# Performance work log

Measured on AMD Instinct MI355X. Metric: run time of the kernel, lower is better.

The kernel has to match this reference:

```python
import jax, jax.numpy as jnp
import numpy as np

IMG_SIZE = 416.0
CLASS_NUM = 80
NUM_ANCH = 3
MAX_GT = 64  # fixed padding for per-image valid GT boxes (original uses a variable-size python loop)


def _bce_logits(x, t):
    # BCEWithLogits, elementwise: softplus(x) - x*t  (numerically stable)
    return jax.nn.softplus(x) - x * t


def _make_noobj_mask(pred_boxes, targets):
    # pred_boxes: [B,G,G,3,4] in pixel units; targets: [B,G,G,3,85]
    B, G = pred_boxes.shape[0], pred_boxes.shape[1]
    N = G * G * NUM_ANCH
    conf = targets[..., 4].reshape(B, N)
    boxes = targets[..., 0:4].reshape(B, N, 4)
    # gather up to MAX_GT ground-truth boxes per image (conf>0 are the valid ones)
    top_conf, idx = jax.lax.top_k(conf, MAX_GT)            # [B,M]
    gt = jnp.take_along_axis(boxes, idx[..., None], axis=1)  # [B,M,4]
    valid = top_conf > 0.0                                   # [B,M]

    p = pred_boxes.reshape(B, N, 4)
    pxy = p[:, :, None, 0:2]   # [B,N,1,2]
    pwh = p[:, :, None, 2:4]
    gxy = gt[:, None, :, 0:2]  # [B,1,M,2]
    gwh = gt[:, None, :, 2:4]

    imin = jnp.maximum(pxy - pwh / 2, gxy - gwh / 2)
    imax = jnp.minimum(pxy + pwh / 2, gxy + gwh / 2)
    iwh = jnp.maximum(imax - imin, 0.0)
    inter = iwh[..., 0] * iwh[..., 1]                        # [B,N,M]
    area_p = pwh[..., 0] * pwh[..., 1]
    area_g = gwh[..., 0] * gwh[..., 1]
    iou = inter / (area_p + area_g - inter + 1e-9)
    iou = jnp.where(valid[:, None, :], iou, 0.0)
    best_iou = jnp.max(iou, axis=-1)                         # [B,N]
    noobj = (best_iou < 0.6).astype(pred_boxes.dtype)
    return noobj.reshape(B, G, G, NUM_ANCH)


def reference(preds, targets, anchors):
    B, G = preds.shape[0], preds.shape[1]
    ratio = IMG_SIZE / G
    p = preds.reshape(B, G, G, NUM_ANCH, 5 + CLASS_NUM)
    box_xy_raw, box_wh_raw, conf_logit, cls_logit = jnp.split(p, [2, 4, 5], axis=-1)

    # grid offsets: offset[i,j] = (j, i)
    gx, gy = jnp.meshgrid(jnp.arange(G, dtype=preds.dtype), jnp.arange(G, dtype=preds.dtype))
    offset = jnp.stack([gx, gy], axis=-1).reshape(G, G, 1, 2)

    sig_xy = jax.nn.sigmoid(box_xy_raw)
    box_xy = (sig_xy + offset) * ratio                 # pixel units
    box_wh = jnp.exp(box_wh_raw) * anchors             # (anchors/ratio)*ratio = anchors
    pred_boxes = jnp.concatenate([box_xy, box_wh], axis=-1)

    preds_xy = box_xy / ratio - offset                 # == sig_xy
    true_xy = targets[..., 0:2] / ratio - offset
    true_wh = targets[..., 2:4] / anchors
    preds_wh = box_wh / anchors
    true_wh = jnp.where(true_wh == 0.0, 1.0, true_wh)
    preds_wh = jnp.where(preds_wh == 0.0, 1.0, preds_wh)
    true_wh = jnp.log(jnp.clip(true_wh, 1e-9, 1e9))
    preds_wh = jnp.log(jnp.clip(preds_wh, 1e-9, 1e9))

    obj = (targets[..., 4] > 0.0).astype(preds.dtype)  # [B,G,G,3]
    obj_e = obj[..., None]
    scale = 2.0 - targets[..., 2:3] / IMG_SIZE * targets[..., 3:4] / IMG_SIZE  # [B,G,G,3,1]

    txty_loss = jnp.sum(obj_e * (preds_xy - true_xy) ** 2 * scale) / B
    twth_loss = jnp.sum(obj_e * (preds_wh - true_wh) ** 2 * scale) / B

    noobj = _make_noobj_mask(pred_boxes, targets)      # [B,G,G,3]
    noobj_conf_mask = (1.0 - obj) * noobj
    conf_t = targets[..., 4:5]
    noobj_conf_loss = jnp.sum(noobj_conf_mask[..., None] * _bce_logits(conf_logit, conf_t)) / B
    obj_conf_loss = jnp.sum(obj_e * _bce_logits(conf_logit, conf_t)) / B
    class_loss = jnp.sum(obj_e * _bce_logits(cls_logit, targets[..., 5:])) / B

    total_loss = txty_loss + twth_loss + noobj_conf_loss + obj_conf_loss + class_loss
    return (txty_loss, twth_loss, noobj_conf_loss, obj_conf_loss, class_loss, total_loss)


def setup_inputs() -> dict:
    key = jax.random.key(0)
    ks = jax.random.split(key, 5)
    B, G, A, C = 32, 52, NUM_ANCH, CLASS_NUM
    N = G * G * A
    M_OBJ = 40  # GT boxes per image (< MAX_GT)
    preds = jax.random.normal(ks[0], (B, G, G, A * (5 + C)), jnp.float32) * 0.5
    idx = jax.random.randint(ks[1], (B, M_OBJ), 0, N)
    xy = jax.random.uniform(ks[2], (B, M_OBJ, 2), jnp.float32, 0.0, IMG_SIZE)
    wh = jax.random.uniform(ks[3], (B, M_OBJ, 2), jnp.float32, 16.0, 128.0)
    cid = jax.random.randint(ks[4], (B, M_OBJ), 0, C)
    onehot = jax.nn.one_hot(cid, C, dtype=jnp.float32)
    vals = jnp.concatenate([xy, wh, jnp.ones((B, M_OBJ, 1), jnp.float32), onehot], axis=-1)
    t = jnp.zeros((B, N, 5 + C), jnp.float32)
    t = t.at[jnp.arange(B)[:, None], idx].set(vals)
    targets = t.reshape(B, G, G, A, 5 + C)
    anchors = jnp.array([[10.0, 13.0], [16.0, 30.0], [33.0, 23.0]], jnp.float32)
    return {"preds": preds, "targets": targets, "anchors": anchors}
```

## Files before the change

### kernel.cpp

```cpp
#include <hip/hip_runtime.h>
#include <math.h>

#define GSZ 52
#define NA 3
#define NCLS 80
#define CH 85
#define NCA (GSZ*GSZ*NA)
#define MAXGT 64
#define RPB 32
#define FPT (RPB*CH)
#define F4PT (FPT/4)
#define MCHUNK 32

__device__ __forceinline__ float softplus_fast(float x) {
    return fmaxf(x, 0.0f) + __logf(1.0f + __expf(-fabsf(x)));
}

__global__ void k_init(int* cnt, int B) {
    if (threadIdx.x < B) cnt[threadIdx.x] = 0;
}

__global__ void k_tp(const float* __restrict__ tg, const float* __restrict__ pr,
                     const float* __restrict__ anchors, int* cnt,
                     float4* __restrict__ gtbox, int2* __restrict__ gtinfo,
                     float4* __restrict__ boxout, float* __restrict__ confout) {
    __shared__ float sT[FPT];
    __shared__ float sP[FPT];
    int tid = threadIdx.x;
    size_t rec0 = (size_t)blockIdx.x * RPB;

    {
        const float4* srcT = (const float4*)(tg + rec0 * CH);
        const float4* srcP = (const float4*)(pr + rec0 * CH);
        float4* dT = (float4*)sT;
        float4* dP = (float4*)sP;
        for (int i = tid; i < F4PT; i += 256) {
            dT[i] = srcT[i];
            dP[i] = srcP[i];
        }
    }
    __syncthreads();

    if (tid < RPB) {
        const float* r = sT + tid * CH;
        float conf = r[4];
        if (conf > 0.0f) {
            size_t glob = rec0 + tid;
            int b    = (int)(glob / NCA);
            int nloc = (int)(glob - (size_t)b * NCA);
            int cid = 0;
            for (int c = 0; c < NCLS; c++) if (r[5 + c] > 0.5f) cid = c;
            int pos = atomicAdd(cnt + b, 1);
            if (pos < MAXGT) {
                gtbox[b * MAXGT + pos]  = make_float4(r[0], r[1], r[2], r[3]);
                gtinfo[b * MAXGT + pos] = make_int2(nloc, cid);
            }
        }
    } else if (tid >= 64 && tid < 64 + RPB) {
        int t = tid - 64;
        const float* r = sP + t * CH;
        size_t glob = rec0 + t;
        int b    = (int)(glob / NCA);
        int nloc = (int)(glob - (size_t)b * NCA);
        int a    = nloc % NA;
        int cell = nloc / NA;
        int gi = cell / GSZ, gj = cell % GSZ;
        float sx = __builtin_amdgcn_rcpf(1.0f + __expf(-r[0]));
        float sy = __builtin_amdgcn_rcpf(1.0f + __expf(-r[1]));
        float ew = __expf(r[2]), eh = __expf(r[3]);
        float aw = anchors[2 * a], ah = anchors[2 * a + 1];
        boxout[glob] = make_float4((sx + (float)gj) * 8.0f,
                                   (sy + (float)gi) * 8.0f,
                                   ew * aw, eh * ah);
        confout[glob] = r[4];
    }
}

__global__ void k_main(const int* __restrict__ cnt,
                       const float4* __restrict__ gtbox,
                       const int2* __restrict__ gtinfo,
                       const float4* __restrict__ boxin,
                       const float* __restrict__ confin,
                       float* __restrict__ partial) {
    __shared__ float4 sbox[MAXGT];
    __shared__ int    sidx[MAXGT];
    __shared__ float  swsum[4];

    int b   = blockIdx.y;
    int tid = threadIdx.x;
    int n   = blockIdx.x * 256 + tid;

    int m = min(cnt[b], MAXGT);
    if (tid < m) {
        sbox[tid] = gtbox[b * MAXGT + tid];
        sidx[tid] = gtinfo[b * MAXGT + tid].x;
    }
    __syncthreads();

    float v = 0.0f;
    if (n < NCA) {
        size_t rec = (size_t)b * NCA + n;
        float4 pb = boxin[rec];
        float  pc = confin[rec];
        float px0 = pb.x - pb.z * 0.5f, px1 = pb.x + pb.z * 0.5f;
        float py0 = pb.y - pb.w * 0.5f, py1 = pb.y + pb.w * 0.5f;
        float areap = pb.z * pb.w;

        float best = 0.0f;
        bool isobj = false;
        for (int k = 0; k < m; k++) {
            float4 g = sbox[k];
            isobj |= (sidx[k] == n);
            float ix = fminf(px1, g.x + g.z * 0.5f) - fmaxf(px0, g.x - g.z * 0.5f);
            float iy = fminf(py1, g.y + g.w * 0.5f) - fmaxf(py0, g.y - g.w * 0.5f);
            float inter = fmaxf(ix, 0.0f) * fmaxf(iy, 0.0f);
            float u = areap + g.z * g.w - inter + 1e-9f;
            best = fmaxf(best, inter * __builtin_amdgcn_rcpf(u));
        }
        if (!isobj && best < 0.6f) v = softplus_fast(pc);
    }

    int lane = tid & 63;
    int wv   = tid >> 6;
    for (int off = 32; off > 0; off >>= 1) v += __shfl_down(v, off);
    if (lane == 0) swsum[wv] = v;
    __syncthreads();
    if (tid == 0) {
        int bid = blockIdx.y * gridDim.x + blockIdx.x;
        partial[bid] = swsum[0] + swsum[1] + swsum[2] + swsum[3];
    }
}

__global__ void k_cls(const float* __restrict__ pr,
                      const float* __restrict__ anchors,
                      const int* __restrict__ cnt,
                      const float4* __restrict__ gtbox,
                      const int2* __restrict__ gtinfo,
                      const float4* __restrict__ boxin,
                      const float* __restrict__ confin,
                      float4* __restrict__ cls4) {
    int tid  = threadIdx.x;
    int wv   = tid >> 6;
    int lane = tid & 63;
    int slot = blockIdx.x * 4 + wv;
    int b = slot >> 6;
    int k = slot & (MAXGT - 1);

    float4 resv = make_float4(0.f, 0.f, 0.f, 0.f);
    int m = min(cnt[b], MAXGT);
    if (k < m) {
        float4 g  = gtbox[slot];
        int2 info = gtinfo[slot];
        int n = info.x, cid = info.y;
        size_t rec = (size_t)b * NCA + n;
        const float* cl = pr + rec * CH + 5;

        float x0 = cl[lane];
        float cls = softplus_fast(x0) - (lane == cid ? x0 : 0.0f);
        if (lane < NCLS - 64) {
            float x1 = cl[64 + lane];
            cls += softplus_fast(x1) - ((64 + lane) == cid ? x1 : 0.0f);
        }
        for (int off = 32; off > 0; off >>= 1) cls += __shfl_down(cls, off);

        if (lane == 0) {
            float4 pb = boxin[rec];
            float  pc = confin[rec];
            int a    = n % NA;
            int cell = n / NA;
            int gi = cell / GSZ, gj = cell % GSZ;
            float aw = anchors[2 * a], ah = anchors[2 * a + 1];

            float scale = 2.0f - (g.z * (1.0f / 416.0f)) * (g.w * (1.0f / 416.0f));
            float dx = (pb.x * 0.125f - (float)gj) - (g.x * 0.125f - (float)gj);
            float dy = (pb.y * 0.125f - (float)gi) - (g.y * 0.125f - (float)gi);
            float txty = (dx * dx + dy * dy) * scale;

            float rw = __builtin_amdgcn_rcpf(aw), rh = __builtin_amdgcn_rcpf(ah);
            float pwr = fminf(fmaxf(pb.z * rw, 1e-9f), 1e9f);
            float phr = fminf(fmaxf(pb.w * rh, 1e-9f), 1e9f);
            float twr = fminf(fmaxf(g.z  * rw, 1e-9f), 1e9f);
            float thr = fminf(fmaxf(g.w  * rh, 1e-9f), 1e9f);
            float dw = __logf(pwr) - __logf(twr);
            float dh = __logf(phr) - __logf(thr);
            float twth = (dw * dw + dh * dh) * scale;

            float obj = softplus_fast(pc) - pc;
            resv = make_float4(txty, twth, obj, cls);
        }
    }
    if (lane == 0) cls4[slot] = resv;
}

__global__ void k_final(const float* __restrict__ partial, int np,
                        const float4* __restrict__ cls4, int ns,
                        int B, float* __restrict__ out) {
    __shared__ double sred[4 * 5];
    int tid = threadIdx.x;
    double acc[5] = {0, 0, 0, 0, 0};
    for (int i = tid; i < np; i += 256) acc[2] += (double)partial[i];
    for (int i = tid; i < ns; i += 256) {
        float4 v = cls4[i];
        acc[0] += (double)v.x; acc[1] += (double)v.y;
        acc[3] += (double)v.z; acc[4] += (double)v.w;
    }
    int lane = tid & 63;
    int wv   = tid >> 6;
#pragma unroll
    for (int i = 0; i < 5; i++) {
        double v = acc[i];
        for (int off = 32; off > 0; off >>= 1) v += __shfl_down(v, off);
        if (lane == 0) sred[wv * 5 + i] = v;
    }
    __syncthreads();
    if (tid == 0) {
        double tot = 0.0;
#pragma unroll
        for (int i = 0; i < 5; i++) {
            double r = (sred[i] + sred[5 + i] + sred[10 + i] + sred[15 + i]) / (double)B;
            out[i] = (float)r;
            tot += r;
        }
        out[5] = (float)tot;
    }
}

extern "C" void kernel_launch(void* const* d_in, const int* in_sizes, int n_in,
                              void* d_out, int out_size, void* d_ws, size_t ws_size,
                              hipStream_t stream) {
    const float* preds   = (const float*)d_in[0];
    const float* targets = (const float*)d_in[1];
    const float* anchors = (const float*)d_in[2];
    float* out = (float*)d_out;

    int B = in_sizes[0] / (NCA * CH);
    size_t total_rec = (size_t)B * NCA;
    int tp_blocks = (int)(total_rec / RPB);
    int np = MCHUNK * B;
    int ns = B * MAXGT;

    char* ws = (char*)d_ws;
    size_t off = 0;
    int*    cnt     = (int*)(ws + off);      off += 128;
    float4* gtbox   = (float4*)(ws + off);   off += (size_t)ns * sizeof(float4);
    int2*   gtinfo  = (int2*)(ws + off);     off += (size_t)ns * sizeof(int2);
    float*  partial = (float*)(ws + off);    off += (size_t)np * sizeof(float);
    off = (off + 15) & ~(size_t)15;
    float4* cls4    = (float4*)(ws + off);   off += (size_t)ns * sizeof(float4);
    float4* boxout  = (float4*)(ws + off);   off += total_rec * sizeof(float4);
    float*  confout = (float*)(ws + off);    off += total_rec * sizeof(float);

    k_init<<<1, 64, 0, stream>>>(cnt, B);
    k_tp<<<tp_blocks, 256, 0, stream>>>(targets, preds, anchors, cnt,
                                        gtbox, gtinfo, boxout, confout);
    dim3 grid(MCHUNK, B);
    k_main<<<grid, 256, 0, stream>>>(cnt, gtbox, gtinfo, boxout, confout, partial);
    k_cls<<<ns / 4, 256, 0, stream>>>(preds, anchors, cnt, gtbox, gtinfo,
                                      boxout, confout, cls4);
    k_final<<<1, 256, 0, stream>>>(partial, np, cls4, ns, B, out);
}
```

Measured before the change: 215.9 us.

## Drop full-tensor staging; read only conf channel and recompute boxes in consumers

The combined transform kernel, which staged every targets and preds record through shared memory, is split up. A new GT-scan kernel reads only the conf channel of targets and touches the full record only for positives. The noobj and class kernels now decode boxes from preds directly, so the intermediate box and conf buffers go away. The aim is to stop streaming both 85-channel tensors in full. The cost is strided 4-byte reads (one per 340-byte record), which use far fewer bytes but make poorly coalesced accesses, plus some duplicated sigmoid and exp work.

```diff
diff --git a/kernel.cpp b/kernel.cpp
--- a/kernel.cpp
+++ b/kernel.cpp
@@ -7,9 +7,6 @@
 #define CH 85
 #define NCA (GSZ*GSZ*NA)
 #define MAXGT 64
-#define RPB 32
-#define FPT (RPB*CH)
-#define F4PT (FPT/4)
 #define MCHUNK 32
 
 __device__ __forceinline__ float softplus_fast(float x) {
@@ -20,68 +17,39 @@
     if (threadIdx.x < B) cnt[threadIdx.x] = 0;
 }
 
-__global__ void k_tp(const float* __restrict__ tg, const float* __restrict__ pr,
-                     const float* __restrict__ anchors, int* cnt,
-                     float4* __restrict__ gtbox, int2* __restrict__ gtinfo,
-                     float4* __restrict__ boxout, float* __restrict__ confout) {
-    __shared__ float sT[FPT];
-    __shared__ float sP[FPT];
+__device__ __forceinline__ void emit_gt(const float* __restrict__ tg, size_t glob,
+                                        int* cnt, float4* __restrict__ gtbox,
+                                        int2* __restrict__ gtinfo) {
+    const float* r = tg + glob * CH;
+    int b    = (int)(glob / NCA);
+    int nloc = (int)(glob - (size_t)b * NCA);
+    int cid = 0;
+#pragma unroll 16
+    for (int c = 0; c < NCLS; c++) if (r[5 + c] > 0.5f) cid = c;
+    int pos = atomicAdd(cnt + b, 1);
+    if (pos < MAXGT) {
+        gtbox[b * MAXGT + pos]  = make_float4(r[0], r[1], r[2], r[3]);
+        gtinfo[b * MAXGT + pos] = make_int2(nloc, cid);
+    }
+}
+
+__global__ void k_gt(const float* __restrict__ tg, int nrec, int* cnt,
+                     float4* __restrict__ gtbox, int2* __restrict__ gtinfo) {
     int tid = threadIdx.x;
-    size_t rec0 = (size_t)blockIdx.x * RPB;
-
-    {
-        const float4* srcT = (const float4*)(tg + rec0 * CH);
-        const float4* srcP = (const float4*)(pr + rec0 * CH);
-        float4* dT = (float4*)sT;
-        float4* dP = (float4*)sP;
-        for (int i = tid; i < F4PT; i += 256) {
-            dT[i] = srcT[i];
-            dP[i] = srcP[i];
-        }
-    }
-    __syncthreads();
-
-    if (tid < RPB) {
-        const float* r = sT + tid * CH;
-        float conf = r[4];
-        if (conf > 0.0f) {
-            size_t glob = rec0 + tid;
-            int b    = (int)(glob / NCA);
-            int nloc = (int)(glob - (size_t)b * NCA);
-            int cid = 0;
-            for (int c = 0; c < NCLS; c++) if (r[5 + c] > 0.5f) cid = c;
-            int pos = atomicAdd(cnt + b, 1);
-            if (pos < MAXGT) {
-                gtbox[b * MAXGT + pos]  = make_float4(r[0], r[1], r[2], r[3]);
-                gtinfo[b * MAXGT + pos] = make_int2(nloc, cid);
-            }
-        }
-    } else if (tid >= 64 && tid < 64 + RPB) {
-        int t = tid - 64;
-        const float* r = sP + t * CH;
-        size_t glob = rec0 + t;
-        int b    = (int)(glob / NCA);
-        int nloc = (int)(glob - (size_t)b * NCA);
-        int a    = nloc % NA;
-        int cell = nloc / NA;
-        int gi = cell / GSZ, gj = cell % GSZ;
-        float sx = __builtin_amdgcn_rcpf(1.0f + __expf(-r[0]));
-        float sy = __builtin_amdgcn_rcpf(1.0f + __expf(-r[1]));
-        float ew = __expf(r[2]), eh = __expf(r[3]);
-        float aw = anchors[2 * a], ah = anchors[2 * a + 1];
-        boxout[glob] = make_float4((sx + (float)gj) * 8.0f,
-                                   (sy + (float)gi) * 8.0f,
-                                   ew * aw, eh * ah);
-        confout[glob] = r[4];
-    }
-}
-
-__global__ void k_main(const int* __restrict__ cnt,
-                       const float4* __restrict__ gtbox,
-                       const int2* __restrict__ gtinfo,
-                       const float4* __restrict__ boxin,
-                       const float* __restrict__ confin,
-                       float* __restrict__ partial) {
+    size_t g0 = (size_t)blockIdx.x * 512 + tid;
+    size_t g1 = g0 + 256;
+    float c0 = (g0 < (size_t)nrec) ? tg[g0 * CH + 4] : 0.0f;
+    float c1 = (g1 < (size_t)nrec) ? tg[g1 * CH + 4] : 0.0f;
+    if (c0 > 0.0f) emit_gt(tg, g0, cnt, gtbox, gtinfo);
+    if (c1 > 0.0f) emit_gt(tg, g1, cnt, gtbox, gtinfo);
+}
+
+__global__ void k_noobj(const float* __restrict__ pr,
+                        const float* __restrict__ anchors,
+                        const int* __restrict__ cnt,
+                        const float4* __restrict__ gtbox,
+                        const int2* __restrict__ gtinfo,
+                        float* __restrict__ partial) {
     __shared__ float4 sbox[MAXGT];
     __shared__ int    sidx[MAXGT];
     __shared__ float  swsum[4];
@@ -99,12 +67,23 @@
 
     float v = 0.0f;
     if (n < NCA) {
-        size_t rec = (size_t)b * NCA + n;
-        float4 pb = boxin[rec];
-        float  pc = confin[rec];
-        float px0 = pb.x - pb.z * 0.5f, px1 = pb.x + pb.z * 0.5f;
-        float py0 = pb.y - pb.w * 0.5f, py1 = pb.y + pb.w * 0.5f;
-        float areap = pb.z * pb.w;
+        const float* r = pr + ((size_t)b * NCA + n) * CH;
+        float r0 = r[0], r1 = r[1], r2 = r[2], r3 = r[3], pc = r[4];
+
+        int a    = n % NA;
+        int cell = n / NA;
+        int gi = cell / GSZ, gj = cell % GSZ;
+        float aw = anchors[2 * a], ah = anchors[2 * a + 1];
+        float sx = __builtin_amdgcn_rcpf(1.0f + __expf(-r0));
+        float sy = __builtin_amdgcn_rcpf(1.0f + __expf(-r1));
+        float bx = (sx + (float)gj) * 8.0f;
+        float by = (sy + (float)gi) * 8.0f;
+        float bw = __expf(r2) * aw;
+        float bh = __expf(r3) * ah;
+
+        float px0 = bx - bw * 0.5f, px1 = bx + bw * 0.5f;
+        float py0 = by - bh * 0.5f, py1 = by + bh * 0.5f;
+        float areap = bw * bh;
 
         float best = 0.0f;
         bool isobj = false;
@@ -136,8 +115,6 @@
                       const int* __restrict__ cnt,
                       const float4* __restrict__ gtbox,
                       const int2* __restrict__ gtinfo,
-                      const float4* __restrict__ boxin,
-                      const float* __restrict__ confin,
                       float4* __restrict__ cls4) {
     int tid  = threadIdx.x;
     int wv   = tid >> 6;
@@ -153,7 +130,8 @@
         int2 info = gtinfo[slot];
         int n = info.x, cid = info.y;
         size_t rec = (size_t)b * NCA + n;
-        const float* cl = pr + rec * CH + 5;
+        const float* rp = pr + rec * CH;
+        const float* cl = rp + 5;
 
         float x0 = cl[lane];
         float cls = softplus_fast(x0) - (lane == cid ? x0 : 0.0f);
@@ -164,21 +142,27 @@
         for (int off = 32; off > 0; off >>= 1) cls += __shfl_down(cls, off);
 
         if (lane == 0) {
-            float4 pb = boxin[rec];
-            float  pc = confin[rec];
+            float r0 = rp[0], r1 = rp[1], r2 = rp[2], r3 = rp[3], pc = rp[4];
             int a    = n % NA;
             int cell = n / NA;
             int gi = cell / GSZ, gj = cell % GSZ;
             float aw = anchors[2 * a], ah = anchors[2 * a + 1];
 
+            float sx = __builtin_amdgcn_rcpf(1.0f + __expf(-r0));
+            float sy = __builtin_amdgcn_rcpf(1.0f + __expf(-r1));
+            float pbx = (sx + (float)gj) * 8.0f;
+            float pby = (sy + (float)gi) * 8.0f;
+            float pbz = __expf(r2) * aw;
+            float pbw = __expf(r3) * ah;
+
             float scale = 2.0f - (g.z * (1.0f / 416.0f)) * (g.w * (1.0f / 416.0f));
-            float dx = (pb.x * 0.125f - (float)gj) - (g.x * 0.125f - (float)gj);
-            float dy = (pb.y * 0.125f - (float)gi) - (g.y * 0.125f - (float)gi);
+            float dx = (pbx * 0.125f - (float)gj) - (g.x * 0.125f - (float)gj);
+            float dy = (pby * 0.125f - (float)gi) - (g.y * 0.125f - (float)gi);
             float txty = (dx * dx + dy * dy) * scale;
 
             float rw = __builtin_amdgcn_rcpf(aw), rh = __builtin_amdgcn_rcpf(ah);
-            float pwr = fminf(fmaxf(pb.z * rw, 1e-9f), 1e9f);
-            float phr = fminf(fmaxf(pb.w * rh, 1e-9f), 1e9f);
+            float pwr = fminf(fmaxf(pbz * rw, 1e-9f), 1e9f);
+            float phr = fminf(fmaxf(pbw * rh, 1e-9f), 1e9f);
             float twr = fminf(fmaxf(g.z  * rw, 1e-9f), 1e9f);
             float thr = fminf(fmaxf(g.w  * rh, 1e-9f), 1e9f);
             float dw = __logf(pwr) - __logf(twr);
@@ -234,8 +218,8 @@
     float* out = (float*)d_out;
 
     int B = in_sizes[0] / (NCA * CH);
-    size_t total_rec = (size_t)B * NCA;
-    int tp_blocks = (int)(total_rec / RPB);
+    int nrec = B * NCA;
+    int gt_blocks = (nrec + 511) / 512;
     int np = MCHUNK * B;
     int ns = B * MAXGT;
 
@@ -247,15 +231,11 @@
     float*  partial = (float*)(ws + off);    off += (size_t)np * sizeof(float);
     off = (off + 15) & ~(size_t)15;
     float4* cls4    = (float4*)(ws + off);   off += (size_t)ns * sizeof(float4);
-    float4* boxout  = (float4*)(ws + off);   off += total_rec * sizeof(float4);
-    float*  confout = (float*)(ws + off);    off += total_rec * sizeof(float);
 
     k_init<<<1, 64, 0, stream>>>(cnt, B);
-    k_tp<<<tp_blocks, 256, 0, stream>>>(targets, preds, anchors, cnt,
-                                        gtbox, gtinfo, boxout, confout);
+    k_gt<<<gt_blocks, 256, 0, stream>>>(targets, nrec, cnt, gtbox, gtinfo);
     dim3 grid(MCHUNK, B);
-    k_main<<<grid, 256, 0, stream>>>(cnt, gtbox, gtinfo, boxout, confout, partial);
-    k_cls<<<ns / 4, 256, 0, stream>>>(preds, anchors, cnt, gtbox, gtinfo,
-                                      boxout, confout, cls4);
+    k_noobj<<<grid, 256, 0, stream>>>(preds, anchors, cnt, gtbox, gtinfo, partial);
+    k_cls<<<ns / 4, 256, 0, stream>>>(preds, anchors, cnt, gtbox, gtinfo, cls4);
     k_final<<<1, 256, 0, stream>>>(partial, np, cls4, ns, B, out);
 }
```

After: 197.1 us. 8.7% less time.
